# Optimization experiments

Hardware: AMD Instinct MI355X
Metric: run time of the kernel (lower is better)

The kernel has to match this reference:

```python
import jax, jax.numpy as jnp
import numpy as np

XZ = jnp.array([0, 2])
XY = jnp.array([0, 1])
YZ = jnp.array([1, 2])


def _bilinear(plane, uv):
    """plane: (C,R,R) as (C,H,W); uv: (N,2) in [0,1], uv[:,0]->width, uv[:,1]->height.
    Border padding + align_corners=True semantics (grid_sample style)."""
    R = plane.shape[-1]
    xy = jnp.clip(uv, 0.0, 1.0) * (R - 1)
    x, y = xy[:, 0], xy[:, 1]
    x0 = jnp.floor(x)
    y0 = jnp.floor(y)
    x0i = jnp.clip(x0.astype(jnp.int32), 0, R - 1)
    y0i = jnp.clip(y0.astype(jnp.int32), 0, R - 1)
    x1i = jnp.clip(x0i + 1, 0, R - 1)
    y1i = jnp.clip(y0i + 1, 0, R - 1)
    wx = (x - x0)[None, :]  # (1,N)
    wy = (y - y0)[None, :]
    f00 = plane[:, y0i, x0i]  # (C,N)
    f01 = plane[:, y0i, x1i]
    f10 = plane[:, y1i, x0i]
    f11 = plane[:, y1i, x1i]
    top = f00 * (1.0 - wx) + f01 * wx
    bot = f10 * (1.0 - wx) + f11 * wx
    return (top * (1.0 - wy) + bot * wy).T  # (N,C)


def _sample_triplane(p, c_xz, c_xy, c_yz):
    """p: (bs,N,3) in [0,1]; planes: (bs,C,R,R). Returns (bs,N,C) summed over planes."""
    def per_batch(pb, fxz, fxy, fyz):
        return (_bilinear(fxz, pb[:, XZ])
                + _bilinear(fxy, pb[:, XY])
                + _bilinear(fyz, pb[:, YZ]))
    return jax.vmap(per_batch)(p, c_xz, c_xy, c_yz)


def setup_inputs() -> dict:
    key = jax.random.key(0)
    ks = jax.random.split(key, 12)
    bs, ns, C, S, R = 2, 50000, 32, 8, 128
    inp = {
        "query_pos": jax.random.uniform(ks[0], (bs, ns, 3), dtype=jnp.float32),
        "c_xz": jax.random.normal(ks[1], (bs, C, R, R), dtype=jnp.float32),
        "c_xy": jax.random.normal(ks[2], (bs, C, R, R), dtype=jnp.float32),
        "c_yz": jax.random.normal(ks[3], (bs, C, R, R), dtype=jnp.float32),
        # offset weights scaled small so sampled points stay mostly in-bounds
        "W_off": jax.random.normal(ks[4], (C, S * 3), dtype=jnp.float32) * 0.01,
        "b_off": jnp.zeros((S * 3,), dtype=jnp.float32),
        "W_w": jax.random.normal(ks[5], (C, S), dtype=jnp.float32) * 0.1,
        "b_w": jnp.zeros((S,), dtype=jnp.float32),
        "W_v": jax.random.normal(ks[6], (C, C), dtype=jnp.float32) * (1.0 / np.sqrt(C)),
        "b_v": jnp.zeros((C,), dtype=jnp.float32),
        "W_out": jax.random.normal(ks[7], (C, C), dtype=jnp.float32) * (1.0 / np.sqrt(C)),
        "b_out": jnp.zeros((C,), dtype=jnp.float32),
    }
    return inp


def reference(query_pos, c_xz, c_xy, c_yz, W_off, b_off, W_w, b_w, W_v, b_v, W_out, b_out):
    bs, ns, _ = query_pos.shape
    S = W_w.shape[1]
    # round 1: sample tri-plane features at query points
    feature = _sample_triplane(query_pos, c_xz, c_xy, c_yz)  # (bs,ns,C)
    # predict per-query sample offsets and weights
    off = (feature @ W_off + b_off).reshape(bs, ns, S, 3)
    w = (feature @ W_w + b_w).reshape(bs, ns, S, 1)
    pts = off + query_pos[:, :, None, :]  # (bs,ns,S,3)
    # round 2: sample at deformed points
    aux = _sample_triplane(pts.reshape(bs, ns * S, 3), c_xz, c_xy, c_yz)
    v = aux.reshape(bs, ns, S, -1) @ W_v + b_v  # (bs,ns,S,C)
    out = (v * w).sum(-2)                        # weighted reduce over samples
    out = out @ W_out + b_out + feature          # residual
    return out  # (bs,ns,C)
```

## Files before the change

### kernel.cpp

```cpp
#include <hip/hip_runtime.h>
#include <hip/hip_fp16.h>

#define BS 2
#define NS 50000
#define CCH 32
#define RR 128
#define SS 8

typedef float v2f __attribute__((ext_vector_type(2)));
typedef _Float16 h2 __attribute__((ext_vector_type(2)));

#if __has_builtin(__builtin_amdgcn_fdot2)
#define HAVE_DOT2 1
#else
#define HAVE_DOT2 0
#endif


__global__ __launch_bounds__(256)
void prep(const float* __restrict__ cxz,
          const float* __restrict__ cxy,
          const float* __restrict__ cyz,
          const float* __restrict__ Wv, const float* __restrict__ bv,
          const float* __restrict__ Wout,
          unsigned* __restrict__ tp, float* __restrict__ Wc,
          float* __restrict__ bvw) {
    __shared__ float lds[32 * 129];
    int tid = threadIdx.x;
    int row = blockIdx.x;
    if (row < BS * 3 * RR) {
        int y  = row & 127;
        int pl = (row >> 7) % 3;
        int b  = row / 384;
        const float* src = (pl == 0) ? cxz : ((pl == 1) ? cxy : cyz);
        const float* sp = src + (((size_t)(b * CCH)) << 14) + (y << 7);
#pragma unroll
        for (int i = 0; i < 16; ++i) {
            int c = (tid >> 7) + 2 * i;
            int x = tid & 127;
            lds[c * 129 + x] = sp[((size_t)c << 14) + x];
        }
        __syncthreads();
        unsigned* dst = tp + ((size_t)row << 12);
#pragma unroll
        for (int i = 0; i < 16; ++i) {
            int idx = tid + 256 * i;
            int c = idx & 31;
            int x = idx >> 5;
            int x1 = min(x + 1, 127);
            unsigned h0 = __half_as_ushort(__float2half(lds[c * 129 + x]));
            unsigned h1 = __half_as_ushort(__float2half(lds[c * 129 + x1]));
            dst[(x << 5) + c] = h0 | (h1 << 16);
        }
    } else {
        int t = (row - BS * 3 * RR) * 256 + tid;
        int c = t >> 5, j = t & 31;
        float acc = 0.f;
#pragma unroll
        for (int k = 0; k < 32; ++k) acc += Wv[c * 32 + k] * Wout[k * 32 + j];
        Wc[t] = acc;
        if (t < 32) {
            float a2 = 0.f;
#pragma unroll
            for (int k = 0; k < 32; ++k) a2 += bv[k] * Wout[k * 32 + t];
            bvw[t] = a2;
        }
    }
}


struct f4 { v2f lo, hi; };

struct Samp { uint4 u[6]; float wc0, wc1, wr1, wr2; };

__device__ __forceinline__ Samp load_samp(const uint4* __restrict__ P0,
                                          float p0, float p1, float p2) {
    Samp t;
    float x0c = fminf(fmaxf(p0, 0.f), 1.f) * 127.f;
    float x1c = fminf(fmaxf(p1, 0.f), 1.f) * 127.f;
    float x2c = fminf(fmaxf(p2, 0.f), 1.f) * 127.f;
    int i0 = min((int)x0c, 126);
    t.wc0 = x0c - (float)i0;
    int i1 = min((int)x1c, 126);
    t.wc1 = x1c - (float)i1;
    float f1 = floorf(x1c);
    int r10 = (int)f1, r11 = min(r10 + 1, 127);
    t.wr1 = x1c - f1;
    float f2 = floorf(x2c);
    int r20 = (int)f2, r21 = min(r20 + 1, 127);
    t.wr2 = x2c - f2;

    const uint4* Pxz = P0;
    const uint4* Pxy = P0 + (1 << 17);
    const uint4* Pyz = P0 + (2 << 17);
    int c0 = i0 << 3, c1 = i1 << 3;
    int R10 = r10 << 10, R11 = r11 << 10;
    int R20 = r20 << 10, R21 = r21 << 10;
    t.u[0] = Pxz[R20 + c0];  t.u[1] = Pxz[R21 + c0];
    t.u[2] = Pxy[R10 + c0];  t.u[3] = Pxy[R11 + c0];
    t.u[4] = Pyz[R20 + c1];  t.u[5] = Pyz[R21 + c1];
    return t;
}

#if HAVE_DOT2
__device__ __forceinline__ void eval_row(f4& acc, uint4 u, h2 w) {
    acc.lo.x = __builtin_amdgcn_fdot2(__builtin_bit_cast(h2, u.x), w, acc.lo.x, false);
    acc.lo.y = __builtin_amdgcn_fdot2(__builtin_bit_cast(h2, u.y), w, acc.lo.y, false);
    acc.hi.x = __builtin_amdgcn_fdot2(__builtin_bit_cast(h2, u.z), w, acc.hi.x, false);
    acc.hi.y = __builtin_amdgcn_fdot2(__builtin_bit_cast(h2, u.w), w, acc.hi.y, false);
}

__device__ __forceinline__ void eval_plane(f4& acc, uint4 ua, uint4 ub,
                                           float wx, float wy) {
    float wB1 = wx * wy;
    float wB0 = wx - wB1;
    float wA1 = wy - wB1;
    float wA0 = 1.f - wx - wA1;
    h2 w0 = __builtin_bit_cast(h2, __builtin_amdgcn_cvt_pkrtz(wA0, wB0));
    h2 w1 = __builtin_bit_cast(h2, __builtin_amdgcn_cvt_pkrtz(wA1, wB1));
    eval_row(acc, ua, w0);
    eval_row(acc, ub, w1);
}
#else
__device__ __forceinline__ void eval_row(f4& acc, uint4 u, float wA, float wB) {
    __half2 h0 = __builtin_bit_cast(__half2, u.x);
    __half2 h1 = __builtin_bit_cast(__half2, u.y);
    __half2 h2_ = __builtin_bit_cast(__half2, u.z);
    __half2 h3 = __builtin_bit_cast(__half2, u.w);
    acc.lo.x = fmaf(__half2float(h0.y), wB, fmaf(__half2float(h0.x), wA, acc.lo.x));
    acc.lo.y = fmaf(__half2float(h1.y), wB, fmaf(__half2float(h1.x), wA, acc.lo.y));
    acc.hi.x = fmaf(__half2float(h2_.y), wB, fmaf(__half2float(h2_.x), wA, acc.hi.x));
    acc.hi.y = fmaf(__half2float(h3.y), wB, fmaf(__half2float(h3.x), wA, acc.hi.y));
}

__device__ __forceinline__ void eval_plane(f4& acc, uint4 ua, uint4 ub,
                                           float wx, float wy) {
    float wB1 = wx * wy;
    float wB0 = wx - wB1;
    float wA1 = wy - wB1;
    float wA0 = 1.f - wx - wA1;
    eval_row(acc, ua, wA0, wB0);
    eval_row(acc, ub, wA1, wB1);
}
#endif

__device__ __forceinline__ void eval_samp(const Samp& t, f4& acc) {
    eval_plane(acc, t.u[0], t.u[1], t.wc0, t.wr2);
    eval_plane(acc, t.u[2], t.u[3], t.wc0, t.wr1);
    eval_plane(acc, t.u[4], t.u[5], t.wc1, t.wr2);
}

#define GETE(v, idx) (((idx) & 2) ? (((idx) & 1) ? (v).hi.y : (v).hi.x) \
                                  : (((idx) & 1) ? (v).lo.y : (v).lo.x))
#define GETC(v, idx) __shfl(GETE(v, idx), base | ((idx) >> 2), 64)

__global__ __launch_bounds__(256)
void eda_main(const float* __restrict__ qp, const unsigned* __restrict__ tp,
              const float* __restrict__ Woff, const float* __restrict__ boff,
              const float* __restrict__ Ww, const float* __restrict__ bw,
              const float* __restrict__ Wc, const float* __restrict__ bvw,
              const float* __restrict__ bout, float* __restrict__ out) {
    __shared__ float sWcat[32][32];
    __shared__ float sWc2[32][32];
    __shared__ float sbcat[32];
    __shared__ float sbvw[32];
    __shared__ float sbout[32];

    int tid = threadIdx.x;
    int lane = tid & 7;
    int base = tid & 56;
    int b  = blockIdx.x & 1;
    int qi = (blockIdx.x >> 1) * 32 + (tid >> 3);
    int qq = min(qi, NS - 1);

    const float* p = qp + ((size_t)b * NS + qq) * 3;
    float p0 = p[0], p1 = p[1], p2 = p[2];

    const uint4* P0 = (const uint4*)tp + (((size_t)(b * 3)) << 17) + lane;

    Samp fs = load_samp(P0, p0, p1, p2);

    for (int i = tid; i < 1024; i += 256) {
        int k = i >> 5, j = i & 31;
        ((float*)sWcat)[i] = (j < 24) ? Woff[k * 24 + j] : Ww[k * 8 + (j - 24)];
        ((float*)sWc2)[i]  = Wc[i];
    }
    if (tid < 32) {
        sbcat[tid] = (tid < 24) ? boff[tid] : bw[tid - 24];
        sbvw[tid]  = bvw[tid];
        sbout[tid] = bout[tid];
    }
    __syncthreads();

    f4 feat; feat.lo = (v2f){0.f, 0.f}; feat.hi = (v2f){0.f, 0.f};
    eval_samp(fs, feat);

    f4 cat;
    cat.lo.x = sbcat[(lane << 2) + 0]; cat.lo.y = sbcat[(lane << 2) + 1];
    cat.hi.x = sbcat[(lane << 2) + 2]; cat.hi.y = sbcat[(lane << 2) + 3];
#pragma unroll
    for (int k = 0; k < 32; ++k) {
        float fc = GETC(feat, k);
        const v2f* wp = (const v2f*)&sWcat[k][lane << 2];
        v2f fc2 = {fc, fc};
        cat.lo = __builtin_elementwise_fma(fc2, wp[0], cat.lo);
        cat.hi = __builtin_elementwise_fma(fc2, wp[1], cat.hi);
    }

    f4 wa; wa.lo = (v2f){0.f, 0.f}; wa.hi = (v2f){0.f, 0.f};
    float wsum = 0.f;
    float w_cur = GETC(cat, 24);
    Samp cur = load_samp(P0, p0 + GETC(cat, 0), p1 + GETC(cat, 1), p2 + GETC(cat, 2));
    Samp nxt;
    float w_nxt;
#pragma unroll
    for (int s = 0; s < SS; ++s) {
        if (s < SS - 1) {
            w_nxt = GETC(cat, 24 + (s + 1));
            nxt = load_samp(P0, p0 + GETC(cat, 3 * (s + 1) + 0),
                                p1 + GETC(cat, 3 * (s + 1) + 1),
                                p2 + GETC(cat, 3 * (s + 1) + 2));
        }
        f4 aux; aux.lo = (v2f){0.f, 0.f}; aux.hi = (v2f){0.f, 0.f};
        eval_samp(cur, aux);
        v2f w2 = {w_cur, w_cur};
        wa.lo = __builtin_elementwise_fma(w2, aux.lo, wa.lo);
        wa.hi = __builtin_elementwise_fma(w2, aux.hi, wa.hi);
        wsum += w_cur;
        if (s < SS - 1) { cur = nxt; w_cur = w_nxt; }
    }

    f4 o;
    v2f ws2 = {wsum, wsum};
    {
        v2f bo  = {sbout[(lane << 2) + 0], sbout[(lane << 2) + 1]};
        v2f bv2 = {sbvw[(lane << 2) + 0], sbvw[(lane << 2) + 1]};
        o.lo = __builtin_elementwise_fma(ws2, bv2, bo) + feat.lo;
        v2f bo2 = {sbout[(lane << 2) + 2], sbout[(lane << 2) + 3]};
        v2f bv3 = {sbvw[(lane << 2) + 2], sbvw[(lane << 2) + 3]};
        o.hi = __builtin_elementwise_fma(ws2, bv3, bo2) + feat.hi;
    }
#pragma unroll
    for (int k = 0; k < 32; ++k) {
        float wc = GETC(wa, k);
        const v2f* wp = (const v2f*)&sWc2[k][lane << 2];
        v2f wc2 = {wc, wc};
        o.lo = __builtin_elementwise_fma(wc2, wp[0], o.lo);
        o.hi = __builtin_elementwise_fma(wc2, wp[1], o.hi);
    }

    if (qi < NS) {
        float* dst = out + ((size_t)b * NS + qi) * 32 + (lane << 2);
        *(float4*)dst = make_float4(o.lo.x, o.lo.y, o.hi.x, o.hi.y);
    }
}

extern "C" void kernel_launch(void* const* d_in, const int* in_sizes, int n_in,
                              void* d_out, int out_size, void* d_ws, size_t ws_size,
                              hipStream_t stream) {
    const float* qp   = (const float*)d_in[0];
    const float* cxz  = (const float*)d_in[1];
    const float* cxy  = (const float*)d_in[2];
    const float* cyz  = (const float*)d_in[3];
    const float* Woff = (const float*)d_in[4];
    const float* boff = (const float*)d_in[5];
    const float* Ww   = (const float*)d_in[6];
    const float* bw   = (const float*)d_in[7];
    const float* Wv   = (const float*)d_in[8];
    const float* bv   = (const float*)d_in[9];
    const float* Wout = (const float*)d_in[10];
    const float* bout = (const float*)d_in[11];
    float* out = (float*)d_out;

    unsigned* tp = (unsigned*)d_ws;
    float* Wc  = (float*)((char*)d_ws + (size_t)BS * 3 * RR * RR * CCH * 4);
    float* bvw = Wc + 1024;

    prep<<<BS * 3 * RR + 4, 256, 0, stream>>>(cxz, cxy, cyz, Wv, bv, Wout, tp, Wc, bvw);
    int blocks_per_batch = (NS + 31) / 32;
    eda_main<<<2 * blocks_per_batch, 256, 0, stream>>>(qp, tp, Woff, boff, Ww, bw,
                                                       Wc, bvw, bout, out);
}
```

Before: 131.8 us.

## Distribute per-sample address and weight math across lanes, fp16 dot2 output projection

The concatenated offset/weight layout is permuted so that each of the 8 lanes of a query owns one sample's (dx,dy,dz,w) in its own registers. Each lane then computes that sample's clamped coordinates, texel offsets and packed fp16 bilinear weights once, instead of every lane redundantly computing them for all 8 samples. The sample loop broadcasts the offsets and packed weights through shuffles. The final W_v·W_out projection now packs its weights and activations to fp16 pairs and uses fdot2, halving its shuffle and FMA count. This lowers precision in that projection and adds shuffles in the sample loop.

```diff
diff --git a/kernel.cpp b/kernel.cpp
--- a/kernel.cpp
+++ b/kernel.cpp
@@ -102,6 +102,15 @@
     return t;
 }
 
+__device__ __forceinline__ unsigned pack2(float a, float b) {
+#if HAVE_DOT2
+    return __builtin_bit_cast(unsigned, __builtin_amdgcn_cvt_pkrtz(a, b));
+#else
+    __half2 h = __floats2half2_rn(a, b);
+    return __builtin_bit_cast(unsigned, h);
+#endif
+}
+
 #if HAVE_DOT2
 __device__ __forceinline__ void eval_row(f4& acc, uint4 u, h2 w) {
     acc.lo.x = __builtin_amdgcn_fdot2(__builtin_bit_cast(h2, u.x), w, acc.lo.x, false);
@@ -121,6 +130,10 @@
     eval_row(acc, ua, w0);
     eval_row(acc, ub, w1);
 }
+
+__device__ __forceinline__ void eval_rowp(f4& acc, uint4 u, unsigned pw) {
+    eval_row(acc, u, __builtin_bit_cast(h2, pw));
+}
 #else
 __device__ __forceinline__ void eval_row(f4& acc, uint4 u, float wA, float wB) {
     __half2 h0 = __builtin_bit_cast(__half2, u.x);
@@ -142,6 +155,11 @@
     eval_row(acc, ua, wA0, wB0);
     eval_row(acc, ub, wA1, wB1);
 }
+
+__device__ __forceinline__ void eval_rowp(f4& acc, uint4 u, unsigned pw) {
+    __half2 hw = __builtin_bit_cast(__half2, pw);
+    eval_row(acc, u, __half2float(hw.x), __half2float(hw.y));
+}
 #endif
 
 __device__ __forceinline__ void eval_samp(const Samp& t, f4& acc) {
@@ -153,6 +171,8 @@
 #define GETE(v, idx) (((idx) & 2) ? (((idx) & 1) ? (v).hi.y : (v).hi.x) \
                                   : (((idx) & 1) ? (v).lo.y : (v).lo.x))
 #define GETC(v, idx) __shfl(GETE(v, idx), base | ((idx) >> 2), 64)
+
+struct SampB { uint4 u[6]; };
 
 __global__ __launch_bounds__(256)
 void eda_main(const float* __restrict__ qp, const unsigned* __restrict__ tp,
@@ -160,8 +180,8 @@
               const float* __restrict__ Ww, const float* __restrict__ bw,
               const float* __restrict__ Wc, const float* __restrict__ bvw,
               const float* __restrict__ bout, float* __restrict__ out) {
-    __shared__ float sWcat[32][32];
-    __shared__ float sWc2[32][32];
+    __shared__ float    sWcat[32][32];
+    __shared__ unsigned sWc2h[16][32];
     __shared__ float sbcat[32];
     __shared__ float sbvw[32];
     __shared__ float sbout[32];
@@ -181,12 +201,17 @@
     Samp fs = load_samp(P0, p0, p1, p2);
 
     for (int i = tid; i < 1024; i += 256) {
-        int k = i >> 5, j = i & 31;
-        ((float*)sWcat)[i] = (j < 24) ? Woff[k * 24 + j] : Ww[k * 8 + (j - 24)];
-        ((float*)sWc2)[i]  = Wc[i];
+        int k = i >> 5, j = i & 31, l2 = j >> 2, e = j & 3;
+        sWcat[k][j] = (e < 3) ? Woff[k * 24 + 3 * l2 + e] : Ww[k * 8 + l2];
+    }
+    {
+        int k2 = tid >> 5, j = tid & 31;
+        sWc2h[k2][j]     = pack2(Wc[k2 * 64 + j],        Wc[k2 * 64 + 32 + j]);
+        sWc2h[k2 + 8][j] = pack2(Wc[(k2 + 8) * 64 + j],  Wc[(k2 + 8) * 64 + 32 + j]);
     }
     if (tid < 32) {
-        sbcat[tid] = (tid < 24) ? boff[tid] : bw[tid - 24];
+        int l2 = tid >> 2, e = tid & 3;
+        sbcat[tid] = (e < 3) ? boff[3 * l2 + e] : bw[l2];
         sbvw[tid]  = bvw[tid];
         sbout[tid] = bout[tid];
     }
@@ -207,27 +232,73 @@
         cat.hi = __builtin_elementwise_fma(fc2, wp[1], cat.hi);
     }
 
+    float sx = p0 + cat.lo.x, sy = p1 + cat.lo.y, sz = p2 + cat.hi.x;
+    float wt_my = cat.hi.y;
+    float x0c = fminf(fmaxf(sx, 0.f), 1.f) * 127.f;
+    int  i0 = min((int)x0c, 126);
+    float wc0 = x0c - (float)i0;
+    float x1c = fminf(fmaxf(sy, 0.f), 1.f) * 127.f;
+    int  i1 = min((int)x1c, 126);
+    float wc1 = x1c - (float)i1;
+    float f1 = floorf(x1c);
+    int r10 = (int)f1, r11 = min(r10 + 1, 127);
+    float wr1 = x1c - f1;
+    float x2c = fminf(fmaxf(sz, 0.f), 1.f) * 127.f;
+    float f2 = floorf(x2c);
+    int r20 = (int)f2, r21 = min(r20 + 1, 127);
+    float wr2 = x2c - f2;
+    int c0 = i0 << 3, c1 = i1 << 3;
+    int o0 = (r20 << 10) + c0;
+    int o1 = (r21 << 10) + c0;
+    int o2 = (1 << 17) + (r10 << 10) + c0;
+    int o3 = (1 << 17) + (r11 << 10) + c0;
+    int o4 = (2 << 17) + (r20 << 10) + c1;
+    int o5 = (2 << 17) + (r21 << 10) + c1;
+    unsigned m0, m1, m2, m3, m4, m5;
+    { float wB1 = wc0 * wr2, wB0 = wc0 - wB1, wA1 = wr2 - wB1, wA0 = 1.f - wc0 - wA1;
+      m0 = pack2(wA0, wB0); m1 = pack2(wA1, wB1); }
+    { float wB1 = wc0 * wr1, wB0 = wc0 - wB1, wA1 = wr1 - wB1, wA0 = 1.f - wc0 - wA1;
+      m2 = pack2(wA0, wB0); m3 = pack2(wA1, wB1); }
+    { float wB1 = wc1 * wr2, wB0 = wc1 - wB1, wA1 = wr2 - wB1, wA0 = 1.f - wc1 - wA1;
+      m4 = pack2(wA0, wB0); m5 = pack2(wA1, wB1); }
+
     f4 wa; wa.lo = (v2f){0.f, 0.f}; wa.hi = (v2f){0.f, 0.f};
     float wsum = 0.f;
-    float w_cur = GETC(cat, 24);
-    Samp cur = load_samp(P0, p0 + GETC(cat, 0), p1 + GETC(cat, 1), p2 + GETC(cat, 2));
-    Samp nxt;
-    float w_nxt;
+    SampB cur, nxt;
+    {
+        int src = base;
+        cur.u[0] = P0[__shfl(o0, src, 64)];
+        cur.u[1] = P0[__shfl(o1, src, 64)];
+        cur.u[2] = P0[__shfl(o2, src, 64)];
+        cur.u[3] = P0[__shfl(o3, src, 64)];
+        cur.u[4] = P0[__shfl(o4, src, 64)];
+        cur.u[5] = P0[__shfl(o5, src, 64)];
+    }
 #pragma unroll
     for (int s = 0; s < SS; ++s) {
         if (s < SS - 1) {
-            w_nxt = GETC(cat, 24 + (s + 1));
-            nxt = load_samp(P0, p0 + GETC(cat, 3 * (s + 1) + 0),
-                                p1 + GETC(cat, 3 * (s + 1) + 1),
-                                p2 + GETC(cat, 3 * (s + 1) + 2));
+            int src = base | (s + 1);
+            nxt.u[0] = P0[__shfl(o0, src, 64)];
+            nxt.u[1] = P0[__shfl(o1, src, 64)];
+            nxt.u[2] = P0[__shfl(o2, src, 64)];
+            nxt.u[3] = P0[__shfl(o3, src, 64)];
+            nxt.u[4] = P0[__shfl(o4, src, 64)];
+            nxt.u[5] = P0[__shfl(o5, src, 64)];
         }
+        int src = base | s;
         f4 aux; aux.lo = (v2f){0.f, 0.f}; aux.hi = (v2f){0.f, 0.f};
-        eval_samp(cur, aux);
-        v2f w2 = {w_cur, w_cur};
+        eval_rowp(aux, cur.u[0], (unsigned)__shfl((int)m0, src, 64));
+        eval_rowp(aux, cur.u[1], (unsigned)__shfl((int)m1, src, 64));
+        eval_rowp(aux, cur.u[2], (unsigned)__shfl((int)m2, src, 64));
+        eval_rowp(aux, cur.u[3], (unsigned)__shfl((int)m3, src, 64));
+        eval_rowp(aux, cur.u[4], (unsigned)__shfl((int)m4, src, 64));
+        eval_rowp(aux, cur.u[5], (unsigned)__shfl((int)m5, src, 64));
+        float wt = __shfl(wt_my, src, 64);
+        v2f w2 = {wt, wt};
         wa.lo = __builtin_elementwise_fma(w2, aux.lo, wa.lo);
         wa.hi = __builtin_elementwise_fma(w2, aux.hi, wa.hi);
-        wsum += w_cur;
-        if (s < SS - 1) { cur = nxt; w_cur = w_nxt; }
+        wsum += wt;
+        if (s < SS - 1) cur = nxt;
     }
 
     f4 o;
@@ -240,13 +311,30 @@
         v2f bv3 = {sbvw[(lane << 2) + 2], sbvw[(lane << 2) + 3]};
         o.hi = __builtin_elementwise_fma(ws2, bv3, bo2) + feat.hi;
     }
-#pragma unroll
-    for (int k = 0; k < 32; ++k) {
-        float wc = GETC(wa, k);
-        const v2f* wp = (const v2f*)&sWc2[k][lane << 2];
-        v2f wc2 = {wc, wc};
-        o.lo = __builtin_elementwise_fma(wc2, wp[0], o.lo);
-        o.hi = __builtin_elementwise_fma(wc2, wp[1], o.hi);
+    unsigned pkLo = pack2(wa.lo.x, wa.lo.y);
+    unsigned pkHi = pack2(wa.hi.x, wa.hi.y);
+#pragma unroll
+    for (int k2 = 0; k2 < 16; ++k2) {
+        unsigned wb = (unsigned)__shfl((int)((k2 & 1) ? pkHi : pkLo), base | (k2 >> 1), 64);
+        const uint4 wv = *(const uint4*)&sWc2h[k2][lane << 2];
+#if HAVE_DOT2
+        h2 wp = __builtin_bit_cast(h2, wb);
+        o.lo.x = __builtin_amdgcn_fdot2(__builtin_bit_cast(h2, wv.x), wp, o.lo.x, false);
+        o.lo.y = __builtin_amdgcn_fdot2(__builtin_bit_cast(h2, wv.y), wp, o.lo.y, false);
+        o.hi.x = __builtin_amdgcn_fdot2(__builtin_bit_cast(h2, wv.z), wp, o.hi.x, false);
+        o.hi.y = __builtin_amdgcn_fdot2(__builtin_bit_cast(h2, wv.w), wp, o.hi.y, false);
+#else
+        __half2 hw = __builtin_bit_cast(__half2, wb);
+        float a0 = __half2float(hw.x), a1 = __half2float(hw.y);
+        __half2 w0 = __builtin_bit_cast(__half2, wv.x);
+        __half2 w1 = __builtin_bit_cast(__half2, wv.y);
+        __half2 w2_ = __builtin_bit_cast(__half2, wv.z);
+        __half2 w3 = __builtin_bit_cast(__half2, wv.w);
+        o.lo.x = fmaf(__half2float(w0.y), a1, fmaf(__half2float(w0.x), a0, o.lo.x));
+        o.lo.y = fmaf(__half2float(w1.y), a1, fmaf(__half2float(w1.x), a0, o.lo.y));
+        o.hi.x = fmaf(__half2float(w2_.y), a1, fmaf(__half2float(w2_.x), a0, o.hi.x));
+        o.hi.y = fmaf(__half2float(w3.y), a1, fmaf(__half2float(w3.x), a0, o.hi.y));
+#endif
     }
 
     if (qi < NS) {
```

After: 129.4 us. No clear change (-1.8%).
